# Performance work log

Hardware: AMD Instinct MI355X
Metric: run time of the kernel (lower is better)

The kernel has to match this reference:

```python
import jax, jax.numpy as jnp
import numpy as np

# Module config (matches init_kwargs)
P_THRESH = 0.9
IOU_THRESH = 0.5
WIDTH, HEIGHT = 3072, 2304
NUM_PATCHES = 96
XPS = WIDTH // NUM_PATCHES   # 32, math.floor(width / num_of_patches)
YPS = HEIGHT // NUM_PATCHES  # 24


def setup_inputs() -> dict:
    key = jax.random.key(0)
    x = jax.random.uniform(key, (5, NUM_PATCHES, NUM_PATCHES), dtype=jnp.float32)
    return {"x": x}


def reference(x):
    """Fixed-shape JAX version of ReduceBoundingBoxes.forward.

    Returns out: [N, 5] rows (score, x, y, w, h) sorted by descending score;
    rows not surviving (prob threshold + greedy NMS) are zeroed.
    (Torch returns only the kept rows; here kept rows appear first, in the
    same order, with identical values, followed by zero rows.)
    """
    P, Q = x.shape[1], x.shape[2]
    N = P * Q
    dt = x.dtype
    ii = (jnp.arange(P, dtype=dt) * XPS)[:, None]  # i * x_patch_size
    jj = (jnp.arange(Q, dtype=dt) * YPS)[None, :]  # j * y_patch_size

    prob = x[0]
    # convert_batch_bbx_to_xyxy_scaled (applied everywhere; only rows passing
    # the prob threshold survive, identical to torch's masked in-place update)
    bx1 = x[1] * WIDTH + ii
    by1 = x[2] * HEIGHT + jj
    bx2 = (x[3] - x[1]) * WIDTH + ii
    by2 = (x[4] - x[2]) * HEIGHT + jj

    boxes = jnp.stack([bx1, by1, bx2, by2], axis=-1).reshape(N, 4)
    scores = prob.reshape(N)
    valid = scores > P_THRESH

    # Sort by descending score; invalid boxes sink to the end.
    order = jnp.argsort(-jnp.where(valid, scores, -jnp.inf))
    boxes_s = boxes[order]
    scores_s = scores[order]
    valid_s = valid[order]

    x1, y1, x2, y2 = boxes_s[:, 0], boxes_s[:, 1], boxes_s[:, 2], boxes_s[:, 3]
    area = (x2 - x1) * (y2 - y1)
    # Pairwise IoU (torchvision convention, no +1). [N, N] -- dominant buffer.
    iw = jnp.clip(jnp.minimum(x2[:, None], x2[None, :]) - jnp.maximum(x1[:, None], x1[None, :]), 0.0)
    ih = jnp.clip(jnp.minimum(y2[:, None], y2[None, :]) - jnp.maximum(y1[:, None], y1[None, :]), 0.0)
    inter = iw * ih
    iou = inter / (area[:, None] + area[None, :] - inter + 1e-9)

    # Greedy NMS: sequential suppression in score order.
    idx = jnp.arange(N)

    def body(i, keep):
        sup = keep[i] & (iou[i] > IOU_THRESH) & (idx > i)
        return keep & ~sup

    keep = jax.lax.fori_loop(0, N, body, valid_s)

    # convert_batch_to_xywh on (score, x1, y1, x2, y2)
    out = jnp.stack([scores_s, x1, y1, x2 - x1, y2 - y1], axis=-1)
    out = jnp.where(keep[:, None], out, jnp.zeros((), dtype=dt))
    return out
```

## Files before the change

### kernel.cpp

```cpp
#pragma clang fp contract(off)
#include <hip/hip_runtime.h>

#define NP 96
#define N_TOT (NP * NP)
#define FWIDTH 3072.0f
#define FHEIGHT 2304.0f
#define XPS 32
#define YPS 24
#define VMAX 1024
typedef unsigned long long u64;

#define WS_MSK   0
#define WS_RANK  131072
#define WS_CNT   135168
#define WS_BX1   135232
#define WS_BY1   139328
#define WS_BX2   143424
#define WS_BY2   147520
#define WS_SSC   151616

__global__ __launch_bounds__(1024)
void k_build(const float* __restrict__ x, float* __restrict__ out,
             u64* __restrict__ msk, unsigned int* __restrict__ grank,
             unsigned int* __restrict__ cntp,
             float* __restrict__ gbx1, float* __restrict__ gby1,
             float* __restrict__ gbx2, float* __restrict__ gby2,
             float* __restrict__ gssc) {
    __shared__ u64 lk[VMAX];
    __shared__ float qx1[VMAX], qy1[VMAX], qx2[VMAX], qy2[VMAX], qa[VMAX];
    __shared__ int part[1024];
    __shared__ unsigned int wcnt[16];

    const int t = threadIdx.x;
    const int lane = t & 63;
    const int wid = t >> 6;
    const int bid = blockIdx.x;

    const int rbase = wid * 576;
    unsigned int cw = 0;
    for (int i = 0; i < 9; ++i) {
        float s = x[rbase + (i << 6) + lane];
        cw += (unsigned int)__popcll(__ballot(s > 0.9f));
    }
    if (lane == 0) wcnt[wid] = cw;
    __syncthreads();
    unsigned int off = 0, tot = 0;
    #pragma unroll
    for (int w = 0; w < 16; ++w) { if (w < wid) off += wcnt[w]; tot += wcnt[w]; }
    const int V = (tot > VMAX) ? VMAX : (int)tot;

    const u64 below = (lane == 0) ? 0ull : (~0ull >> (64 - lane));
    unsigned int base = off;
    for (int i = 0; i < 9; ++i) {
        const int n = rbase + (i << 6) + lane;
        const float s = x[n];
        const bool v = s > 0.9f;
        const u64 m = __ballot(v ? 1 : 0);
        if (v) {
            unsigned int pos = base + (unsigned int)__popcll(m & below);
            if (pos < VMAX) {
                unsigned int bits = __float_as_uint(s);
                lk[pos] = ((u64)(~bits) << 32) | (unsigned int)n;
            }
        }
        base += (unsigned int)__popcll(m);
    }
    for (int i = V + t; i < VMAX; i += 1024) lk[i] = ~0ULL;
    __syncthreads();

    {
        float bx1 = 0.f, by1 = 0.f, bx2 = 0.f, by2 = 0.f, ar = 0.f;
        if (t < V) {
            u64 key = lk[t];
            unsigned int n = (unsigned int)(key & 0xffffffffu);
            int pi = (int)n / NP, pj = (int)n % NP;
            float fi = (float)(pi * XPS);
            float fj = (float)(pj * YPS);
            float v1 = x[1 * N_TOT + n];
            float v2 = x[2 * N_TOT + n];
            float v3 = x[3 * N_TOT + n];
            float v4 = x[4 * N_TOT + n];
            bx1 = __fadd_rn(__fmul_rn(v1, FWIDTH), fi);
            by1 = __fadd_rn(__fmul_rn(v2, FHEIGHT), fj);
            bx2 = __fadd_rn(__fmul_rn(__fsub_rn(v3, v1), FWIDTH), fi);
            by2 = __fadd_rn(__fmul_rn(__fsub_rn(v4, v2), FHEIGHT), fj);
            ar  = __fmul_rn(__fsub_rn(bx2, bx1), __fsub_rn(by2, by1));
        }
        qx1[t] = bx1; qy1[t] = by1; qx2[t] = bx2; qy2[t] = by2; qa[t] = ar;
    }
    const int p = (bid << 6) + lane;
    const u64 colkey = lk[p];
    {
        int c = 0;
        const int sb = wid << 6;
        #pragma unroll 8
        for (int k = 0; k < 64; ++k)
            c += (lk[sb + k] < colkey) ? 1 : 0;
        part[t] = c;
    }
    __syncthreads();

    {
        const float bx1 = qx1[p], by1 = qy1[p], bx2 = qx2[p], by2 = qy2[p], ba = qa[p];
        const int ib = wid << 6;
        u64 bits = 0ull;
        #pragma unroll 4
        for (int m = 0; m < 64; ++m) {
            const int im = ib + m;
            float iw = fmaxf(__fsub_rn(fminf(qx2[im], bx2), fmaxf(qx1[im], bx1)), 0.0f);
            float ih = fmaxf(__fsub_rn(fminf(qy2[im], by2), fmaxf(qy1[im], by1)), 0.0f);
            float inter = __fmul_rn(iw, ih);
            float denom = __fadd_rn(__fsub_rn(__fadd_rn(qa[im], ba), inter), 1e-9f);
            bool pred = (lk[im] < colkey) && ((inter / denom) > 0.5f);
            bits |= ((u64)(pred ? 1u : 0u)) << m;
        }
        msk[(wid << 10) + p] = bits;
    }
    if (t < 64 && p < V) {
        int rank = 0;
        #pragma unroll
        for (int sg = 0; sg < 16; ++sg) rank += part[lane + (sg << 6)];
        grank[p] = (unsigned int)rank;
    }
    {
        const int gt = (bid << 10) + t;
        for (int i = VMAX * 5 + gt; i < N_TOT * 5; i += 16384) out[i] = 0.0f;
    }
    if (bid == 0) {
        if (t == 0) *cntp = (unsigned int)V;
        gbx1[t] = qx1[t];
        gby1[t] = qy1[t];
        gbx2[t] = qx2[t];
        gby2[t] = qy2[t];
        gssc[t] = __uint_as_float(~(unsigned int)(lk[t] >> 32));
    }
}

__global__ __launch_bounds__(1024)
void k_resolve(const unsigned int* __restrict__ cntp,
               const u64* __restrict__ msk, const unsigned int* __restrict__ grank,
               const float* __restrict__ gbx1, const float* __restrict__ gby1,
               const float* __restrict__ gbx2, const float* __restrict__ gby2,
               const float* __restrict__ gssc, float* __restrict__ out) {
    __shared__ u64 savail[16], sD[16];
    const int t = threadIdx.x;
    const int lane = t & 63;
    const int wid = t >> 6;
    const int V = (int)*cntp;
    const bool valid = (t < V);

    const float x1 = gbx1[t], y1 = gby1[t], x2 = gbx2[t], y2 = gby2[t], sc = gssc[t];
    u64 colw[16];
    #pragma unroll
    for (int c = 0; c < 16; ++c)
        colw[c] = msk[(c << 10) + t];

    u64 w0 = __ballot(valid ? 1 : 0);
    if (lane == 0) savail[wid] = w0;
    __syncthreads();

    bool kept = false;
    for (;;) {
        u64 av[16]; u64 any = 0ull;
        #pragma unroll
        for (int c = 0; c < 16; ++c) { av[c] = savail[c]; any |= av[c]; }
        if (any == 0ull) break;
        const bool in_avail = valid && ((av[wid] >> lane) & 1ull);
        u64 conf = 0ull;
        #pragma unroll
        for (int c = 0; c < 16; ++c) conf |= (colw[c] & av[c]);
        const bool isD = in_avail && (conf == 0ull);
        u64 Dw = __ballot(isD ? 1 : 0);
        if (lane == 0) sD[wid] = Dw;
        __syncthreads();
        u64 confD = 0ull;
        #pragma unroll
        for (int c = 0; c < 16; ++c) confD |= (colw[c] & sD[c]);
        if (isD) kept = true;
        const bool drop = in_avail && (isD || confD != 0ull);
        u64 dropw = __ballot(drop ? 1 : 0);
        if (lane == 0) savail[wid] = av[wid] & ~dropw;
        __syncthreads();
    }

    if (valid) {
        unsigned int r = grank[t];
        float o0 = 0.f, o1 = 0.f, o2 = 0.f, o3 = 0.f, o4 = 0.f;
        if (kept) {
            o0 = sc;
            o1 = x1;
            o2 = y1;
            o3 = __fsub_rn(x2, x1);
            o4 = __fsub_rn(y2, y1);
        }
        out[r * 5 + 0] = o0;
        out[r * 5 + 1] = o1;
        out[r * 5 + 2] = o2;
        out[r * 5 + 3] = o3;
        out[r * 5 + 4] = o4;
    } else {
        out[t * 5 + 0] = 0.f;
        out[t * 5 + 1] = 0.f;
        out[t * 5 + 2] = 0.f;
        out[t * 5 + 3] = 0.f;
        out[t * 5 + 4] = 0.f;
    }
}

extern "C" void kernel_launch(void* const* d_in, const int* in_sizes, int n_in,
                              void* d_out, int out_size, void* d_ws, size_t ws_size,
                              hipStream_t stream) {
    const float* x = (const float*)d_in[0];
    float* out = (float*)d_out;
    char* ws = (char*)d_ws;
    u64*          msk   = (u64*)(ws + WS_MSK);
    unsigned int* grank = (unsigned int*)(ws + WS_RANK);
    unsigned int* cnt   = (unsigned int*)(ws + WS_CNT);
    float* gbx1 = (float*)(ws + WS_BX1);
    float* gby1 = (float*)(ws + WS_BY1);
    float* gbx2 = (float*)(ws + WS_BX2);
    float* gby2 = (float*)(ws + WS_BY2);
    float* gssc = (float*)(ws + WS_SSC);

    hipLaunchKernelGGL(k_build,   dim3(16), dim3(1024), 0, stream,
                       x, out, msk, grank, cnt, gbx1, gby1, gbx2, gby2, gssc);
    hipLaunchKernelGGL(k_resolve, dim3(1),  dim3(1024), 0, stream,
                       cnt, msk, grank, gbx1, gby1, gbx2, gby2, gssc, out);
}
```

Before: 79.70 us.

## Split mask-build kernel into 64 blocks of 256 threads

Relaunches the IoU mask builder as 64 blocks of 256 threads instead of 16 blocks of 1024, so each block handles 16 columns instead of 64 and the work spreads across more compute units. The per-block compaction loop now scans 36 chunks per wave, and box setup and the global copy are striped over 4 iterations. Every block still redundantly reads and compacts the full score plane, so the duplicated prologue grows relative to useful work. The resolve kernel also hoists its rank load ahead of the loop.

```diff
diff --git a/kernel.cpp b/kernel.cpp
--- a/kernel.cpp
+++ b/kernel.cpp
@@ -19,7 +19,7 @@
 #define WS_BY2   147520
 #define WS_SSC   151616
 
-__global__ __launch_bounds__(1024)
+__global__ __launch_bounds__(256)
 void k_build(const float* __restrict__ x, float* __restrict__ out,
              u64* __restrict__ msk, unsigned int* __restrict__ grank,
              unsigned int* __restrict__ cntp,
@@ -28,17 +28,17 @@
              float* __restrict__ gssc) {
     __shared__ u64 lk[VMAX];
     __shared__ float qx1[VMAX], qy1[VMAX], qx2[VMAX], qy2[VMAX], qa[VMAX];
-    __shared__ int part[1024];
-    __shared__ unsigned int wcnt[16];
+    __shared__ int part[256];
+    __shared__ unsigned int wcnt[4];
 
     const int t = threadIdx.x;
     const int lane = t & 63;
     const int wid = t >> 6;
     const int bid = blockIdx.x;
 
-    const int rbase = wid * 576;
+    const int rbase = wid * 2304;
     unsigned int cw = 0;
-    for (int i = 0; i < 9; ++i) {
+    for (int i = 0; i < 36; ++i) {
         float s = x[rbase + (i << 6) + lane];
         cw += (unsigned int)__popcll(__ballot(s > 0.9f));
     }
@@ -46,12 +46,12 @@
     __syncthreads();
     unsigned int off = 0, tot = 0;
     #pragma unroll
-    for (int w = 0; w < 16; ++w) { if (w < wid) off += wcnt[w]; tot += wcnt[w]; }
+    for (int w = 0; w < 4; ++w) { if (w < wid) off += wcnt[w]; tot += wcnt[w]; }
     const int V = (tot > VMAX) ? VMAX : (int)tot;
 
     const u64 below = (lane == 0) ? 0ull : (~0ull >> (64 - lane));
     unsigned int base = off;
-    for (int i = 0; i < 9; ++i) {
+    for (int i = 0; i < 36; ++i) {
         const int n = rbase + (i << 6) + lane;
         const float s = x[n];
         const bool v = s > 0.9f;
@@ -65,13 +65,15 @@
         }
         base += (unsigned int)__popcll(m);
     }
-    for (int i = V + t; i < VMAX; i += 1024) lk[i] = ~0ULL;
-    __syncthreads();
-
-    {
+    for (int i = V + t; i < VMAX; i += 256) lk[i] = ~0ULL;
+    __syncthreads();
+
+    #pragma unroll
+    for (int i = 0; i < 4; ++i) {
+        const int idx = t + (i << 8);
         float bx1 = 0.f, by1 = 0.f, bx2 = 0.f, by2 = 0.f, ar = 0.f;
-        if (t < V) {
-            u64 key = lk[t];
+        if (idx < V) {
+            u64 key = lk[idx];
             unsigned int n = (unsigned int)(key & 0xffffffffu);
             int pi = (int)n / NP, pj = (int)n % NP;
             float fi = (float)(pi * XPS);
@@ -86,23 +88,28 @@
             by2 = __fadd_rn(__fmul_rn(__fsub_rn(v4, v2), FHEIGHT), fj);
             ar  = __fmul_rn(__fsub_rn(bx2, bx1), __fsub_rn(by2, by1));
         }
-        qx1[t] = bx1; qy1[t] = by1; qx2[t] = bx2; qy2[t] = by2; qa[t] = ar;
-    }
-    const int p = (bid << 6) + lane;
-    const u64 colkey = lk[p];
+        qx1[idx] = bx1; qy1[idx] = by1; qx2[idx] = bx2; qy2[idx] = by2; qa[idx] = ar;
+    }
     {
+        const int cl  = t & 15;
+        const int seg = t >> 4;
+        const u64 ck = lk[(bid << 4) + cl];
         int c = 0;
-        const int sb = wid << 6;
+        const int sb = seg << 6;
         #pragma unroll 8
         for (int k = 0; k < 64; ++k)
-            c += (lk[sb + k] < colkey) ? 1 : 0;
+            c += (lk[sb + k] < ck) ? 1 : 0;
         part[t] = c;
     }
     __syncthreads();
 
     {
-        const float bx1 = qx1[p], by1 = qy1[p], bx2 = qx2[p], by2 = qy2[p], ba = qa[p];
-        const int ib = wid << 6;
+        const int jl = t & 15;
+        const int w  = t >> 4;
+        const int j  = (bid << 4) + jl;
+        const u64 colkey = lk[j];
+        const float bx1 = qx1[j], by1 = qy1[j], bx2 = qx2[j], by2 = qy2[j], ba = qa[j];
+        const int ib = w << 6;
         u64 bits = 0ull;
         #pragma unroll 4
         for (int m = 0; m < 64; ++m) {
@@ -114,25 +121,32 @@
             bool pred = (lk[im] < colkey) && ((inter / denom) > 0.5f);
             bits |= ((u64)(pred ? 1u : 0u)) << m;
         }
-        msk[(wid << 10) + p] = bits;
-    }
-    if (t < 64 && p < V) {
-        int rank = 0;
-        #pragma unroll
-        for (int sg = 0; sg < 16; ++sg) rank += part[lane + (sg << 6)];
-        grank[p] = (unsigned int)rank;
+        msk[(w << 10) + j] = bits;
+    }
+    if (t < 16) {
+        const int p = (bid << 4) + t;
+        if (p < V) {
+            int rank = 0;
+            #pragma unroll
+            for (int sg = 0; sg < 16; ++sg) rank += part[(sg << 4) + t];
+            grank[p] = (unsigned int)rank;
+        }
     }
     {
-        const int gt = (bid << 10) + t;
+        const int gt = (bid << 8) + t;
         for (int i = VMAX * 5 + gt; i < N_TOT * 5; i += 16384) out[i] = 0.0f;
     }
     if (bid == 0) {
         if (t == 0) *cntp = (unsigned int)V;
-        gbx1[t] = qx1[t];
-        gby1[t] = qy1[t];
-        gbx2[t] = qx2[t];
-        gby2[t] = qy2[t];
-        gssc[t] = __uint_as_float(~(unsigned int)(lk[t] >> 32));
+        #pragma unroll
+        for (int i = 0; i < 4; ++i) {
+            const int idx = t + (i << 8);
+            gbx1[idx] = qx1[idx];
+            gby1[idx] = qy1[idx];
+            gbx2[idx] = qx2[idx];
+            gby2[idx] = qy2[idx];
+            gssc[idx] = __uint_as_float(~(unsigned int)(lk[idx] >> 32));
+        }
     }
 }
 
@@ -150,6 +164,7 @@
     const bool valid = (t < V);
 
     const float x1 = gbx1[t], y1 = gby1[t], x2 = gbx2[t], y2 = gby2[t], sc = gssc[t];
+    const unsigned int r = grank[t];
     u64 colw[16];
     #pragma unroll
     for (int c = 0; c < 16; ++c)
@@ -184,7 +199,6 @@
     }
 
     if (valid) {
-        unsigned int r = grank[t];
         float o0 = 0.f, o1 = 0.f, o2 = 0.f, o3 = 0.f, o4 = 0.f;
         if (kept) {
             o0 = sc;
@@ -222,7 +236,7 @@
     float* gby2 = (float*)(ws + WS_BY2);
     float* gssc = (float*)(ws + WS_SSC);
 
-    hipLaunchKernelGGL(k_build,   dim3(16), dim3(1024), 0, stream,
+    hipLaunchKernelGGL(k_build,   dim3(64), dim3(256),  0, stream,
                        x, out, msk, grank, cnt, gbx1, gby1, gbx2, gby2, gssc);
     hipLaunchKernelGGL(k_resolve, dim3(1),  dim3(1024), 0, stream,
                        cnt, msk, grank, gbx1, gby1, gbx2, gby2, gssc, out);
```

Result: no change. 80.19 us (+0.6%).
